# Kernel tuning notes

Measured on AMD Instinct MI355X. Metric: run time of the kernel, lower is better.

The kernel has to match this reference:

```python
import jax, jax.numpy as jnp
import numpy as np

N_NODES = 100000
N_EDGES = 1600000
DIM_IN = 165
DIM_HID = 128


def setup_inputs() -> dict:
    key = jax.random.key(0)
    ks = jax.random.split(key, 8)
    x = jax.random.normal(ks[0], (N_NODES, DIM_IN), dtype=jnp.float32)
    edge_index = jax.random.randint(ks[1], (2, N_EDGES), 0, N_NODES, dtype=jnp.int64)
    s1 = 1.0 / np.sqrt(DIM_IN)
    s2 = 1.0 / np.sqrt(DIM_HID)
    # PyG GraphConv: lin_rel (with bias) applied to aggregated neighbors,
    # lin_root (no bias) applied to self features.
    W_rel1 = jax.random.uniform(ks[2], (DIM_HID, DIM_IN), jnp.float32, -s1, s1)
    b_rel1 = jax.random.uniform(ks[3], (DIM_HID,), jnp.float32, -s1, s1)
    W_root1 = jax.random.uniform(ks[4], (DIM_HID, DIM_IN), jnp.float32, -s1, s1)
    W_rel2 = jax.random.uniform(ks[5], (1, DIM_HID), jnp.float32, -s2, s2)
    b_rel2 = jax.random.uniform(ks[6], (1,), jnp.float32, -s2, s2)
    W_root2 = jax.random.uniform(ks[7], (1, DIM_HID), jnp.float32, -s2, s2)
    return {"x": x, "edge_index": edge_index,
            "W_rel1": W_rel1, "b_rel1": b_rel1, "W_root1": W_root1,
            "W_rel2": W_rel2, "b_rel2": b_rel2, "W_root2": W_root2}


def _graph_conv(x, src, dst, W_rel, b_rel, W_root):
    # agg[i] = sum_{(j->i) in E} x[j]  (add aggregation, source_to_target flow)
    agg = jax.ops.segment_sum(x[src], dst, num_segments=N_NODES)
    return agg @ W_rel.T + b_rel + x @ W_root.T


def reference(x, edge_index, W_rel1, b_rel1, W_root1, W_rel2, b_rel2, W_root2):
    src, dst = edge_index[0], edge_index[1]
    h = _graph_conv(x, src, dst, W_rel1, b_rel1, W_root1)
    h = jax.nn.relu(h)
    # dropout p=0.1 is identity in eval mode (deterministic reference)
    out = _graph_conv(h, src, dst, W_rel2, b_rel2, W_root2)
    return jax.nn.sigmoid(out)  # [N_NODES, 1]
```

## Files before the change

### kernel.cpp

```cpp
#include <hip/hip_runtime.h>
#include <hip/hip_bf16.h>
#include <math.h>

#define N_NODES 100000
#define N_EDGES 1600000
#define DIM_IN 165
#define DIM_HID 128
#define K_PAD 192
#define NBUCK 391
#define EPB 16384
#define NHB 98
#define CAP 6144

typedef __attribute__((ext_vector_type(8))) short short8v;
typedef __attribute__((ext_vector_type(4))) float f32x4;

__global__ void k_detect(const int* __restrict__ e32, int* __restrict__ flag,
                         int* __restrict__ gcount) {
    int t = threadIdx.x;
    if (t == 0) {
        int z = 0;
        for (int k = 0; k < 16; ++k) z |= e32[2 * k + 1];
        flag[0] = (z == 0) ? 1 : 0;
    }
    if (t < NBUCK) gcount[t] = 0;
}

__global__ void k_histB(const int* __restrict__ e32, const int* __restrict__ flag,
                        int* __restrict__ gcount, int* __restrict__ blockBase) {
    __shared__ int lc[NBUCK];
    int t = threadIdx.x;
    for (int i = t; i < NBUCK; i += 256) lc[i] = 0;
    __syncthreads();
    int isI64 = flag[0];
    int base = blockIdx.x * EPB;
    int lim = base + EPB; if (lim > N_EDGES) lim = N_EDGES;
    const long long* e64 = (const long long*)e32;
    for (int i = base + t; i < lim; i += 256) {
        int d = isI64 ? (int)e64[N_EDGES + i] : e32[N_EDGES + i];
        atomicAdd(&lc[d >> 8], 1);
    }
    __syncthreads();
    for (int b = t; b < NBUCK; b += 256)
        blockBase[blockIdx.x * NBUCK + b] = atomicAdd(&gcount[b], lc[b]);
}

__global__ void k_scanb(const int* __restrict__ gcount, int* __restrict__ bucketStart,
                        int* __restrict__ row_ptr) {
    __shared__ int s[512];
    int t = threadIdx.x;
    s[t] = (t < NBUCK) ? gcount[t] : 0;
    __syncthreads();
    for (int o = 1; o < 512; o <<= 1) {
        int v = s[t]; int a = (t >= o) ? s[t - o] : 0;
        __syncthreads(); s[t] = v + a; __syncthreads();
    }
    if (t < NBUCK) bucketStart[t + 1] = s[t];
    if (t == 0) { bucketStart[0] = 0; row_ptr[N_NODES] = N_EDGES; }
}

__global__ void k_scatterB(const int* __restrict__ e32, const int* __restrict__ flag,
                           const int* __restrict__ bucketStart, const int* __restrict__ blockBase,
                           int2* __restrict__ pairs) {
    __shared__ int lcur[NBUCK];
    int t = threadIdx.x;
    for (int b = t; b < NBUCK; b += 256)
        lcur[b] = bucketStart[b] + blockBase[blockIdx.x * NBUCK + b];
    __syncthreads();
    int isI64 = flag[0];
    int base = blockIdx.x * EPB;
    int lim = base + EPB; if (lim > N_EDGES) lim = N_EDGES;
    const long long* e64 = (const long long*)e32;
    for (int i = base + t; i < lim; i += 256) {
        int s, d;
        if (isI64) { s = (int)e64[i]; d = (int)e64[N_EDGES + i]; }
        else       { s = e32[i];      d = e32[N_EDGES + i]; }
        int pos = atomicAdd(&lcur[d >> 8], 1);
        pairs[pos] = make_int2(s, d);
    }
}

__global__ void k_sortB(const int2* __restrict__ pairs, const int* __restrict__ bucketStart,
                        int* __restrict__ row_ptr, int* __restrict__ esrc) {
    __shared__ int srcb[CAP];
    __shared__ int cnt[256];
    __shared__ int scn[256];
    int t = threadIdx.x;
    int b = blockIdx.x;
    int s0 = bucketStart[b], s1 = bucketStart[b + 1];
    int n = s1 - s0; if (n > CAP) n = CAP;
    cnt[t] = 0;
    __syncthreads();
    for (int i = t; i < n; i += 256) {
        int2 p = pairs[s0 + i];
        int ld = p.y & 255;
        srcb[i] = p.x | (ld << 20);
        atomicAdd(&cnt[ld], 1);
    }
    __syncthreads();
    scn[t] = cnt[t];
    __syncthreads();
    for (int o = 1; o < 256; o <<= 1) {
        int v = scn[t]; int a = (t >= o) ? scn[t - o] : 0;
        __syncthreads(); scn[t] = v + a; __syncthreads();
    }
    int excl = scn[t] - cnt[t];
    int node = b * 256 + t;
    if (node < N_NODES) row_ptr[node] = s0 + excl;
    __syncthreads();
    cnt[t] = excl;
    __syncthreads();
    for (int i = t; i < n; i += 256) {
        int v = srcb[i];
        int ld = v >> 20;
        int r = atomicAdd(&cnt[ld], 1);
        esrc[s0 + r] = v & 0xFFFFF;
    }
}

__global__ void k_prepw(const float* __restrict__ Wrel1, const float* __restrict__ Wroot1,
                        unsigned short* __restrict__ Wpk) {
    int idx = blockIdx.x * 256 + threadIdx.x;
    if (idx < (K_PAD / 8) * 256 * 8) {
        int j = idx & 7;
        int n = (idx >> 3) & 255;
        int p = idx >> 11;
        int k = p * 8 + j;
        float v = 0.f;
        if (k < DIM_IN) v = (n < 128) ? Wrel1[n * DIM_IN + k] : Wroot1[(n - 128) * DIM_IN + k];
        unsigned u = __float_as_uint(v);
        u += 0x7FFFu + ((u >> 16) & 1u);
        Wpk[idx] = (unsigned short)(u >> 16);
    }
}

__launch_bounds__(256, 4)
__global__ void k_gemm_mfma(const float* __restrict__ x, const unsigned short* __restrict__ Wpk,
                            unsigned short* __restrict__ y_rel, float* __restrict__ y_root) {
    __shared__ unsigned short lh[32][232];
    __shared__ unsigned short ll[32][232];
    int tid = threadIdx.x;
    int base = blockIdx.x * 32;

    const float4* xg = (const float4*)(x + (size_t)base * DIM_IN);
    for (int i = tid; i < 1320; i += 256) {
        float4 v = xg[i];
        int fi = i * 4;
        #pragma unroll
        for (int e = 0; e < 4; ++e) {
            int idx = fi + e;
            int r = idx / DIM_IN;
            int k = idx - r * DIM_IN;
            float f = (e == 0) ? v.x : (e == 1) ? v.y : (e == 2) ? v.z : v.w;
            unsigned u = __float_as_uint(f);
            unsigned short hi = (unsigned short)(u >> 16);
            float fhi = __uint_as_float(u & 0xFFFF0000u);
            float lo = f - fhi;
            unsigned short lob = (unsigned short)(__float_as_uint(lo) >> 16);
            lh[r][k] = hi;
            ll[r][k] = lob;
        }
    }
    for (int i = tid; i < 32 * (K_PAD - DIM_IN); i += 256) {
        int r = i / (K_PAD - DIM_IN);
        int k = DIM_IN + (i - r * (K_PAD - DIM_IN));
        lh[r][k] = 0; ll[r][k] = 0;
    }
    __syncthreads();

    int w = tid >> 6, l = tid & 63;
    int rowg = w & 1;
    int colh = w >> 1;
    int m = l & 15, kg = l >> 4;
    int arow = rowg * 16 + m;

    f32x4 acc[8];
    #pragma unroll
    for (int t = 0; t < 8; ++t) acc[t] = (f32x4){0.f, 0.f, 0.f, 0.f};

    const short8v* ap_h = (const short8v*)(&lh[arow][0]);
    const short8v* ap_l = (const short8v*)(&ll[arow][0]);
    const short8v* bp   = (const short8v*)Wpk;
    int bidx = kg * 256 + colh * 128 + m;

    #pragma unroll
    for (int kc = 0; kc < 6; ++kc) {
        short8v ah = ap_h[kc * 4 + kg];
        short8v al = ap_l[kc * 4 + kg];
        short8v bfrag[8];
        #pragma unroll
        for (int t = 0; t < 8; ++t) bfrag[t] = bp[bidx + kc * 1024 + t * 16];
        #pragma unroll
        for (int t = 0; t < 8; ++t)
            acc[t] = __builtin_amdgcn_mfma_f32_16x16x32_bf16(ah, bfrag[t], acc[t], 0, 0, 0);
        #pragma unroll
        for (int t = 0; t < 8; ++t)
            acc[t] = __builtin_amdgcn_mfma_f32_16x16x32_bf16(al, bfrag[t], acc[t], 0, 0, 0);
    }

    int orow = base + rowg * 16 + kg * 4;
    if (colh == 0) {
        #pragma unroll
        for (int t = 0; t < 8; ++t) {
            #pragma unroll
            for (int q = 0; q < 4; ++q) {
                unsigned u = __float_as_uint(acc[t][q]);
                u += 0x7FFFu + ((u >> 16) & 1u);
                y_rel[(size_t)(orow + q) * 128 + t * 16 + m] = (unsigned short)(u >> 16);
            }
        }
    } else {
        #pragma unroll
        for (int t = 0; t < 8; ++t) {
            #pragma unroll
            for (int q = 0; q < 4; ++q)
                y_root[(size_t)(orow + q) * 128 + t * 16 + m] = acc[t][q];
        }
    }
}

__launch_bounds__(256, 2)
__global__ void k_agg(const unsigned short* __restrict__ y_rel, const float* __restrict__ y_root,
                      const int* __restrict__ row_ptr, const int* __restrict__ esrc,
                      const float* __restrict__ b_rel1, const float* __restrict__ W_rel2,
                      const float* __restrict__ W_root2,
                      float* __restrict__ s_out, float* __restrict__ r_out) {
    int node = blockIdx.x * 4 + (threadIdx.x >> 6);
    int lane = threadIdx.x & 63;
    const unsigned* yr = (const unsigned*)y_rel;
    int e0 = row_ptr[node], e1 = row_ptr[node + 1];
    float ax0 = 0.f, ay0 = 0.f, ax1 = 0.f, ay1 = 0.f;
    float ax2 = 0.f, ay2 = 0.f, ax3 = 0.f, ay3 = 0.f;
    int e = e0;
    for (; e + 3 < e1; e += 4) {
        int s0 = esrc[e], s1 = esrc[e + 1], s2 = esrc[e + 2], s3 = esrc[e + 3];
        unsigned v0 = yr[(size_t)s0 * 64 + lane];
        unsigned v1 = yr[(size_t)s1 * 64 + lane];
        unsigned v2 = yr[(size_t)s2 * 64 + lane];
        unsigned v3 = yr[(size_t)s3 * 64 + lane];
        ax0 += __uint_as_float(v0 << 16); ay0 += __uint_as_float(v0 & 0xFFFF0000u);
        ax1 += __uint_as_float(v1 << 16); ay1 += __uint_as_float(v1 & 0xFFFF0000u);
        ax2 += __uint_as_float(v2 << 16); ay2 += __uint_as_float(v2 & 0xFFFF0000u);
        ax3 += __uint_as_float(v3 << 16); ay3 += __uint_as_float(v3 & 0xFFFF0000u);
    }
    for (; e < e1; ++e) {
        unsigned v0 = yr[(size_t)esrc[e] * 64 + lane];
        ax0 += __uint_as_float(v0 << 16); ay0 += __uint_as_float(v0 & 0xFFFF0000u);
    }
    float ax = (ax0 + ax1) + (ax2 + ax3);
    float ay = (ay0 + ay1) + (ay2 + ay3);

    float2 b2 = ((const float2*)b_rel1)[lane];
    float2 rt = ((const float2*)y_root)[(size_t)node * 64 + lane];
    float hx = ax + b2.x + rt.x; hx = hx > 0.f ? hx : 0.f;
    float hy = ay + b2.y + rt.y; hy = hy > 0.f ? hy : 0.f;
    float2 wr2 = ((const float2*)W_rel2)[lane];
    float2 wo2 = ((const float2*)W_root2)[lane];
    float sd = fmaf(hx, wr2.x, hy * wr2.y);
    float rd = fmaf(hx, wo2.x, hy * wo2.y);
    #pragma unroll
    for (int o = 32; o > 0; o >>= 1) {
        sd += __shfl_down(sd, o);
        rd += __shfl_down(rd, o);
    }
    if (lane == 0) { s_out[node] = sd; r_out[node] = rd; }
}

__global__ void k_final(const float* __restrict__ s_in, const float* __restrict__ r_in,
                        const int* __restrict__ row_ptr, const int* __restrict__ esrc,
                        const float* __restrict__ b_rel2, float* __restrict__ out) {
    int i = blockIdx.x * blockDim.x + threadIdx.x;
    if (i < N_NODES) {
        int e0 = row_ptr[i], e1 = row_ptr[i + 1];
        float sum = 0.f;
        for (int e = e0; e < e1; ++e) sum += s_in[esrc[e]];
        float z = sum + b_rel2[0] + r_in[i];
        out[i] = 1.f / (1.f + expf(-z));
    }
}

extern "C" void kernel_launch(void* const* d_in, const int* in_sizes, int n_in,
                              void* d_out, int out_size, void* d_ws, size_t ws_size,
                              hipStream_t stream) {
    const float* x      = (const float*)d_in[0];
    const int*   eidx   = (const int*)d_in[1];
    const float* Wrel1  = (const float*)d_in[2];
    const float* brel1  = (const float*)d_in[3];
    const float* Wroot1 = (const float*)d_in[4];
    const float* Wrel2  = (const float*)d_in[5];
    const float* brel2  = (const float*)d_in[6];
    const float* Wroot2 = (const float*)d_in[7];
    float* out = (float*)d_out;

    char* basep = (char*)d_ws;
    size_t off = 0;
    auto alloc = [&](size_t bytes) -> void* {
        off = (off + 511) & ~(size_t)511;
        void* r = basep + off;
        off += bytes;
        return r;
    };
    int*   flag        = (int*)alloc(4);
    unsigned short* Wpk = (unsigned short*)alloc((size_t)(K_PAD / 8) * 256 * 8 * 2);
    int*   row_ptr     = (int*)alloc((size_t)(N_NODES + 1) * 4);
    int*   esrc        = (int*)alloc((size_t)N_EDGES * 4);
    float* s_buf       = (float*)alloc((size_t)N_NODES * 4);
    float* r_buf       = (float*)alloc((size_t)N_NODES * 4);
    int*   bucketStart = (int*)alloc((size_t)(NBUCK + 1) * 4);
    int*   gcount      = (int*)alloc((size_t)NBUCK * 4);
    size_t union_base = (off + 511) & ~(size_t)511;
    off = union_base;
    int2*  pairs     = (int2*)alloc((size_t)N_EDGES * 8);
    int*   blockBase = (int*)alloc((size_t)NHB * NBUCK * 4);
    off = union_base;
    unsigned short* y_rel  = (unsigned short*)alloc((size_t)N_NODES * DIM_HID * 2);
    float*          y_root = (float*)alloc((size_t)N_NODES * DIM_HID * 4);

    hipLaunchKernelGGL(k_detect,   dim3(1),     dim3(512), 0, stream, eidx, flag, gcount);
    hipLaunchKernelGGL(k_histB,    dim3(NHB),   dim3(256), 0, stream, eidx, flag, gcount, blockBase);
    hipLaunchKernelGGL(k_scanb,    dim3(1),     dim3(512), 0, stream, gcount, bucketStart, row_ptr);
    hipLaunchKernelGGL(k_scatterB, dim3(NHB),   dim3(256), 0, stream, eidx, flag, bucketStart, blockBase, pairs);
    hipLaunchKernelGGL(k_sortB,    dim3(NBUCK), dim3(256), 0, stream, pairs, bucketStart, row_ptr, esrc);
    hipLaunchKernelGGL(k_prepw,    dim3(192),   dim3(256), 0, stream, Wrel1, Wroot1, Wpk);
    hipLaunchKernelGGL(k_gemm_mfma,dim3(3125),  dim3(256), 0, stream, x, Wpk, y_rel, y_root);
    hipLaunchKernelGGL(k_agg,      dim3(25000), dim3(256), 0, stream, y_rel, y_root, row_ptr, esrc,
                       brel1, Wrel2, Wroot2, s_buf, r_buf);
    hipLaunchKernelGGL(k_final,    dim3(391),   dim3(256), 0, stream, s_buf, r_buf, row_ptr, esrc,
                       brel2, out);
}
```

Before: 314.9 us.

## Widen aggregation gathers to 16-byte loads and use wave-per-node final reduction

```diff
diff --git a/kernel.cpp b/kernel.cpp
--- a/kernel.cpp
+++ b/kernel.cpp
@@ -219,7 +219,7 @@
     }
 }
 
-__launch_bounds__(256, 2)
+__launch_bounds__(256, 8)
 __global__ void k_agg(const unsigned short* __restrict__ y_rel, const float* __restrict__ y_root,
                       const int* __restrict__ row_ptr, const int* __restrict__ esrc,
                       const float* __restrict__ b_rel1, const float* __restrict__ W_rel2,
@@ -227,55 +227,85 @@
                       float* __restrict__ s_out, float* __restrict__ r_out) {
     int node = blockIdx.x * 4 + (threadIdx.x >> 6);
     int lane = threadIdx.x & 63;
-    const unsigned* yr = (const unsigned*)y_rel;
+    int li = lane & 15;
+    int qid = lane >> 4;
+    const uint4* yr = (const uint4*)y_rel;
+
     int e0 = row_ptr[node], e1 = row_ptr[node + 1];
-    float ax0 = 0.f, ay0 = 0.f, ax1 = 0.f, ay1 = 0.f;
-    float ax2 = 0.f, ay2 = 0.f, ax3 = 0.f, ay3 = 0.f;
-    int e = e0;
-    for (; e + 3 < e1; e += 4) {
-        int s0 = esrc[e], s1 = esrc[e + 1], s2 = esrc[e + 2], s3 = esrc[e + 3];
-        unsigned v0 = yr[(size_t)s0 * 64 + lane];
-        unsigned v1 = yr[(size_t)s1 * 64 + lane];
-        unsigned v2 = yr[(size_t)s2 * 64 + lane];
-        unsigned v3 = yr[(size_t)s3 * 64 + lane];
-        ax0 += __uint_as_float(v0 << 16); ay0 += __uint_as_float(v0 & 0xFFFF0000u);
-        ax1 += __uint_as_float(v1 << 16); ay1 += __uint_as_float(v1 & 0xFFFF0000u);
-        ax2 += __uint_as_float(v2 << 16); ay2 += __uint_as_float(v2 & 0xFFFF0000u);
-        ax3 += __uint_as_float(v3 << 16); ay3 += __uint_as_float(v3 & 0xFFFF0000u);
-    }
-    for (; e < e1; ++e) {
-        unsigned v0 = yr[(size_t)esrc[e] * 64 + lane];
-        ax0 += __uint_as_float(v0 << 16); ay0 += __uint_as_float(v0 & 0xFFFF0000u);
-    }
-    float ax = (ax0 + ax1) + (ax2 + ax3);
-    float ay = (ay0 + ay1) + (ay2 + ay3);
-
-    float2 b2 = ((const float2*)b_rel1)[lane];
-    float2 rt = ((const float2*)y_root)[(size_t)node * 64 + lane];
-    float hx = ax + b2.x + rt.x; hx = hx > 0.f ? hx : 0.f;
-    float hy = ay + b2.y + rt.y; hy = hy > 0.f ? hy : 0.f;
-    float2 wr2 = ((const float2*)W_rel2)[lane];
-    float2 wo2 = ((const float2*)W_root2)[lane];
-    float sd = fmaf(hx, wr2.x, hy * wr2.y);
-    float rd = fmaf(hx, wo2.x, hy * wo2.y);
-    #pragma unroll
-    for (int o = 32; o > 0; o >>= 1) {
-        sd += __shfl_down(sd, o);
-        rd += __shfl_down(rd, o);
+    float a0 = 0.f, a1 = 0.f, a2 = 0.f, a3 = 0.f;
+    float a4 = 0.f, a5 = 0.f, a6 = 0.f, a7 = 0.f;
+
+    for (int eb = e0; eb < e1; eb += 64) {
+        int cnt = e1 - eb; if (cnt > 64) cnt = 64;
+        int ed = (eb + lane < e1) ? esrc[eb + lane] : 0;
+        int kfull = cnt & ~3;
+        for (int k = 0; k < kfull; k += 4) {
+            int src = __shfl(ed, k + qid);
+            uint4 v = yr[(size_t)src * 16 + li];
+            a0 += __uint_as_float(v.x << 16); a1 += __uint_as_float(v.x & 0xFFFF0000u);
+            a2 += __uint_as_float(v.y << 16); a3 += __uint_as_float(v.y & 0xFFFF0000u);
+            a4 += __uint_as_float(v.z << 16); a5 += __uint_as_float(v.z & 0xFFFF0000u);
+            a6 += __uint_as_float(v.w << 16); a7 += __uint_as_float(v.w & 0xFFFF0000u);
+        }
+        if (kfull < cnt) {
+            int src = __shfl(ed, (kfull + qid < cnt) ? (kfull + qid) : kfull);
+            if (kfull + qid < cnt) {
+                uint4 v = yr[(size_t)src * 16 + li];
+                a0 += __uint_as_float(v.x << 16); a1 += __uint_as_float(v.x & 0xFFFF0000u);
+                a2 += __uint_as_float(v.y << 16); a3 += __uint_as_float(v.y & 0xFFFF0000u);
+                a4 += __uint_as_float(v.z << 16); a5 += __uint_as_float(v.z & 0xFFFF0000u);
+                a6 += __uint_as_float(v.w << 16); a7 += __uint_as_float(v.w & 0xFFFF0000u);
+            }
+        }
+    }
+    #pragma unroll
+    for (int o = 16; o <= 32; o <<= 1) {
+        a0 += __shfl_xor(a0, o); a1 += __shfl_xor(a1, o);
+        a2 += __shfl_xor(a2, o); a3 += __shfl_xor(a3, o);
+        a4 += __shfl_xor(a4, o); a5 += __shfl_xor(a5, o);
+        a6 += __shfl_xor(a6, o); a7 += __shfl_xor(a7, o);
+    }
+
+    const float4* bb = (const float4*)(b_rel1 + 8 * li);
+    const float4* rt = (const float4*)(y_root + (size_t)node * 128 + 8 * li);
+    const float4* w2 = (const float4*)(W_rel2 + 8 * li);
+    const float4* wo = (const float4*)(W_root2 + 8 * li);
+    float4 b0 = bb[0], b1 = bb[1];
+    float4 r0 = rt[0], r1 = rt[1];
+    float4 p0 = w2[0], p1 = w2[1];
+    float4 q0 = wo[0], q1 = wo[1];
+    float h0 = fmaxf(a0 + b0.x + r0.x, 0.f), h1 = fmaxf(a1 + b0.y + r0.y, 0.f);
+    float h2 = fmaxf(a2 + b0.z + r0.z, 0.f), h3 = fmaxf(a3 + b0.w + r0.w, 0.f);
+    float h4 = fmaxf(a4 + b1.x + r1.x, 0.f), h5 = fmaxf(a5 + b1.y + r1.y, 0.f);
+    float h6 = fmaxf(a6 + b1.z + r1.z, 0.f), h7 = fmaxf(a7 + b1.w + r1.w, 0.f);
+    float sd = h0 * p0.x + h1 * p0.y + h2 * p0.z + h3 * p0.w
+             + h4 * p1.x + h5 * p1.y + h6 * p1.z + h7 * p1.w;
+    float rd = h0 * q0.x + h1 * q0.y + h2 * q0.z + h3 * q0.w
+             + h4 * q1.x + h5 * q1.y + h6 * q1.z + h7 * q1.w;
+    #pragma unroll
+    for (int o = 1; o <= 8; o <<= 1) {
+        sd += __shfl_xor(sd, o);
+        rd += __shfl_xor(rd, o);
     }
     if (lane == 0) { s_out[node] = sd; r_out[node] = rd; }
 }
 
+__launch_bounds__(256, 8)
 __global__ void k_final(const float* __restrict__ s_in, const float* __restrict__ r_in,
                         const int* __restrict__ row_ptr, const int* __restrict__ esrc,
                         const float* __restrict__ b_rel2, float* __restrict__ out) {
-    int i = blockIdx.x * blockDim.x + threadIdx.x;
-    if (i < N_NODES) {
-        int e0 = row_ptr[i], e1 = row_ptr[i + 1];
-        float sum = 0.f;
-        for (int e = e0; e < e1; ++e) sum += s_in[esrc[e]];
-        float z = sum + b_rel2[0] + r_in[i];
-        out[i] = 1.f / (1.f + expf(-z));
+    int node = blockIdx.x * 4 + (threadIdx.x >> 6);
+    int lane = threadIdx.x & 63;
+    int e0 = row_ptr[node], e1 = row_ptr[node + 1];
+    float sum = 0.f;
+    for (int eb = e0; eb < e1; eb += 64) {
+        if (eb + lane < e1) sum += s_in[esrc[eb + lane]];
+    }
+    #pragma unroll
+    for (int o = 1; o <= 32; o <<= 1) sum += __shfl_xor(sum, o);
+    if (lane == 0) {
+        float z = sum + b_rel2[0] + r_in[node];
+        out[node] = 1.f / (1.f + expf(-z));
     }
 }
 
@@ -325,6 +355,6 @@
     hipLaunchKernelGGL(k_gemm_mfma,dim3(3125),  dim3(256), 0, stream, x, Wpk, y_rel, y_root);
     hipLaunchKernelGGL(k_agg,      dim3(25000), dim3(256), 0, stream, y_rel, y_root, row_ptr, esrc,
                        brel1, Wrel2, Wroot2, s_buf, r_buf);
-    hipLaunchKernelGGL(k_final,    dim3(391),   dim3(256), 0, stream, s_buf, r_buf, row_ptr, esrc,
+    hipLaunchKernelGGL(k_final,    dim3(25000), dim3(256), 0, stream, s_buf, r_buf, row_ptr, esrc,
                        brel2, out);
 }
```

After: 324.1 us. +2.9%, slower.
